# Performance work log

Measured on AMD Instinct MI355X. Metric: run time of the kernel, lower is better.

## Reference

```python
import jax, jax.numpy as jnp
import numpy as np

BN_EPS = 1e-5

def _bn_eval(x, gamma, beta):
    # Fresh torch BatchNorm1d in eval mode: running_mean=0, running_var=1
    return x * (gamma / jnp.sqrt(1.0 + BN_EPS)) + beta

def setup_inputs() -> dict:
    key = jax.random.key(0)
    ks = jax.random.split(key, 10)
    Q, K, H, W, D = 64, 128, 24, 8, 128
    L = H * W            # seq_len = 192
    FF = 2048            # dim_feedforward
    q_feat = jax.random.normal(ks[0], (Q, H, W, D), dtype=jnp.float32)
    g_feat = jax.random.normal(ks[1], (K, H, W, D), dtype=jnp.float32)
    se = jax.random.normal(ks[2], (L, L), dtype=jnp.float32)
    score_embed = (se + se.T).reshape(1, 1, L, L)
    s = 1.0 / np.sqrt(D)
    fc0_w = jax.random.uniform(ks[3], (D, D), jnp.float32, -s, s)
    fc0_b = jax.random.uniform(ks[4], (D,), jnp.float32, -s, s)
    s2 = 1.0 / np.sqrt(L)
    fc2_w = jax.random.uniform(ks[5], (FF, L), jnp.float32, -s2, s2)
    fc2_b = jax.random.uniform(ks[6], (FF,), jnp.float32, -s2, s2)
    s3 = 1.0 / np.sqrt(FF)
    fc3_w = jax.random.uniform(ks[7], (1, FF), jnp.float32, -s3, s3)
    fc3_b = jax.random.uniform(ks[8], (1,), jnp.float32, -s3, s3)
    bn1_g = jnp.ones((1,)); bn1_b = jnp.zeros((1,))
    bn2_g = jnp.ones((FF,)) + 0.1 * jax.random.normal(ks[9], (FF,), jnp.float32)
    bn2_b = jnp.zeros((FF,))
    bn3_g = jnp.ones((1,)); bn3_b = jnp.zeros((1,))
    return dict(q_feat=q_feat, g_feat=g_feat, score_embed=score_embed,
                fc0_w=fc0_w, fc0_b=fc0_b, fc2_w=fc2_w, fc2_b=fc2_b,
                fc3_w=fc3_w, fc3_b=fc3_b, bn1_g=bn1_g, bn1_b=bn1_b,
                bn2_g=bn2_g, bn2_b=bn2_b, bn3_g=bn3_g, bn3_b=bn3_b)

def reference(q_feat, g_feat, score_embed, fc0_w, fc0_b, fc2_w, fc2_b,
              fc3_w, fc3_b, bn1_g, bn1_b, bn2_g, bn2_b, bn3_g, bn3_b):
    Q = q_feat.shape[0]
    K = g_feat.shape[0]
    D = q_feat.shape[-1]
    L = score_embed.shape[-1]  # seq_len
    tgt = q_feat.reshape(Q, L, D)
    mem = g_feat.reshape(K, L, D)
    query = tgt @ fc0_w.T + fc0_b      # [Q, L, D]
    key_ = mem @ fc0_w.T + fc0_b       # [K, L, D]
    # [Q, K, L(s), L(t)] score, modulated by broadcast sigmoid bias
    score = jnp.einsum('qtd,ksd->qkst', query, key_) * jax.nn.sigmoid(score_embed)
    score = score.reshape(Q * K, L, L)
    # max over s and over t, concatenated per pair -> [QK, 2L]
    score = jnp.concatenate([score.max(axis=1), score.max(axis=2)], axis=-1)
    score = score.reshape(-1, L)       # [2*QK, L]
    score = _bn_eval(score, bn1_g, bn1_b)
    score = score @ fc2_w.T + fc2_b    # [2*QK, FF]
    score = _bn_eval(score, bn2_g, bn2_b)
    score = jax.nn.relu(score)
    score = score @ fc3_w.T + fc3_b    # [2*QK, 1]
    score = score.reshape(-1, 2).sum(axis=-1, keepdims=True)  # [QK, 1]
    score = _bn_eval(score, bn3_g, bn3_b)
    return score.reshape(Q, K)
```

## Files before the change

kernel.cpp:

```cpp
#include <hip/hip_runtime.h>

#define LL 192
#define FF 2048

typedef __attribute__((__ext_vector_type__(8)))  __bf16 bf16x8;
typedef __attribute__((__ext_vector_type__(4)))  __bf16 bf16x4;
typedef __attribute__((__ext_vector_type__(4)))  float  f32x4;

#define MFMA16(a, b, c) __builtin_amdgcn_mfma_f32_16x16x32_bf16((a), (b), (c), 0, 0, 0)


__launch_bounds__(256, 2)
__global__ void proj_prep_kernel(const float* __restrict__ qf_in,
                                 const float* __restrict__ gf_in,
                                 const float* __restrict__ fc0w,
                                 const float* __restrict__ fc0b,
                                 const float* __restrict__ se,
                                 const float* __restrict__ fc2w,
                                 const float* __restrict__ fc2b,
                                 const float* __restrict__ bn2g,
                                 const float* __restrict__ bn2b,
                                 const float* __restrict__ fc3w,
                                 __bf16* __restrict__ kfragA,
                                 __bf16* __restrict__ qfrag16,
                                 __bf16* __restrict__ sig16,
                                 __bf16* __restrict__ fc2w_bf,
                                 float* __restrict__ h2,
                                 float* __restrict__ bb2,
                                 float* __restrict__ f3)
{
    int bx = blockIdx.x, tid = threadIdx.x;
    if (bx >= 1152) {
        int i0 = (bx - 1152) * 256 + tid;
        const int stride = 160 * 256;
        const float c1 = rsqrtf(1.f + 1e-5f);
        for (int i = i0; i < LL * LL; i += stride) {
            int r = i & 3, lane = (i >> 2) & 63, tile = i >> 8;
            int jt = tile % 12, st = tile / 12;
            int s = st * 16 + (lane >> 4) * 4 + r;
            int t = jt * 16 + (lane & 15);
            sig16[i] = (__bf16)(1.f / (1.f + __expf(-se[s * 192 + t])));
        }
        for (int i = i0; i < FF * LL; i += stride)
            fc2w_bf[i] = (__bf16)fc2w[i];
        for (int i = i0; i < FF; i += stride) {
            float h = bn2g[i] * c1;
            h2[i]  = h;
            bb2[i] = fc2b[i] * h + bn2b[i];
            f3[i]  = fc3w[i];
        }
        return;
    }
    __shared__ __bf16 Xs[32][136];
    __shared__ __bf16 Ws[128][136];
    __shared__ __bf16 Os[4096];
    const float* src = (bx < 384) ? (qf_in + (size_t)bx * (32 * 128))
                                  : (gf_in + (size_t)(bx - 384) * (32 * 128));
#pragma unroll
    for (int it = 0; it < 4; ++it) {
        int e = (it * 256 + tid) * 4;
        int r = e >> 7, c = e & 127;
        float4 v = *reinterpret_cast<const float4*>(src + e);
        bf16x4 xv;
        xv[0] = (__bf16)v.x; xv[1] = (__bf16)v.y;
        xv[2] = (__bf16)v.z; xv[3] = (__bf16)v.w;
        *reinterpret_cast<bf16x4*>(&Xs[r][c]) = xv;
    }
#pragma unroll
    for (int it = 0; it < 16; ++it) {
        int e = (it * 256 + tid) * 4;
        int r = e >> 7, c = e & 127;
        float4 v = *reinterpret_cast<const float4*>(fc0w + e);
        bf16x4 xv;
        xv[0] = (__bf16)v.x; xv[1] = (__bf16)v.y;
        xv[2] = (__bf16)v.z; xv[3] = (__bf16)v.w;
        *reinterpret_cast<bf16x4*>(&Ws[r][c]) = xv;
    }
    __syncthreads();

    int wv = tid >> 6, lane = tid & 63, quad = lane >> 4, l16 = lane & 15;
    int n0 = wv * 32;
    f32x4 acc[2][2];
#pragma unroll
    for (int m = 0; m < 2; ++m)
#pragma unroll
        for (int n = 0; n < 2; ++n) acc[m][n] = (f32x4){0.f, 0.f, 0.f, 0.f};
#pragma unroll
    for (int ks = 0; ks < 4; ++ks) {
        bf16x8 a0 = *reinterpret_cast<const bf16x8*>(&Xs[l16][ks * 32 + quad * 8]);
        bf16x8 a1 = *reinterpret_cast<const bf16x8*>(&Xs[16 + l16][ks * 32 + quad * 8]);
        bf16x8 b0 = *reinterpret_cast<const bf16x8*>(&Ws[n0 + l16][ks * 32 + quad * 8]);
        bf16x8 b1 = *reinterpret_cast<const bf16x8*>(&Ws[n0 + 16 + l16][ks * 32 + quad * 8]);
        acc[0][0] = MFMA16(a0, b0, acc[0][0]);
        acc[0][1] = MFMA16(a0, b1, acc[0][1]);
        acc[1][0] = MFMA16(a1, b0, acc[1][0]);
        acc[1][1] = MFMA16(a1, b1, acc[1][1]);
    }
#pragma unroll
    for (int mt = 0; mt < 2; ++mt)
#pragma unroll
        for (int nt = 0; nt < 2; ++nt) {
            int d = n0 + nt * 16 + l16;
            float bv = fc0b[d];
            int abase = mt * 2048 + (d >> 5) * 512 + ((d >> 3) & 3) * 128 + (d & 7);
#pragma unroll
            for (int r = 0; r < 4; ++r)
                Os[abase + (quad * 4 + r) * 8] = (__bf16)(acc[mt][nt][r] + bv);
        }
    __syncthreads();

    int row0 = bx * 32;
    __bf16* dst;
    if (bx < 384) {
        int qi = row0 / 192, tg0 = (row0 % 192) >> 4;
        dst = qfrag16 + qi * 24576 + tg0 * 2048;
    } else {
        int rk0 = row0 - 12288;
        int ki = rk0 / 192, sg0 = (rk0 % 192) >> 4;
        dst = kfragA + ki * 24576 + sg0 * 2048;
    }
#pragma unroll
    for (int it = 0; it < 2; ++it) {
        int e = (it * 256 + tid) * 8;
        *reinterpret_cast<bf16x8*>(dst + e) =
            *reinterpret_cast<const bf16x8*>(&Os[e]);
    }
}

__launch_bounds__(256, 2)
__global__ void score_kernel(const __bf16* __restrict__ kfragA,
                             const __bf16* __restrict__ qfrag16,
                             const __bf16* __restrict__ sig16,
                             const float* __restrict__ bn1g,
                             const float* __restrict__ bn1b,
                             __bf16* __restrict__ Sred)
{
    __shared__ __bf16 Abuf[12288];
    __shared__ __bf16 rowT4[16][200];

    int tid = threadIdx.x;
    int q = blockIdx.x & 63;
    int kbase = (blockIdx.x >> 6) << 3;
    int w = tid >> 6, lane = tid & 63, quad = lane >> 4, l16 = lane & 15;
    const float g1c = bn1g[0] * rsqrtf(1.f + 1e-5f);
    const float b1v = bn1b[0];

    bf16x8 Bf[3][4];
    {
        const __bf16* qb = qfrag16 + (size_t)q * 24576 + lane * 8;
#pragma unroll
        for (int j = 0; j < 3; ++j)
#pragma unroll
            for (int ks = 0; ks < 4; ++ks)
                Bf[j][ks] = *reinterpret_cast<const bf16x8*>(
                    qb + ((3 * w + j) * 4 + ks) * 512);
    }

#pragma unroll 1
    for (int kk = 0; kk < 8; ++kk) {
        int kidx = kbase + kk;
        const __bf16* kp = kfragA + (size_t)kidx * 24576;
        size_t ob = (size_t)(q * 128 + kidx) * 384;
        float cm0 = -3.0e38f, cm1 = -3.0e38f, cm2 = -3.0e38f;

#pragma unroll 1
        for (int h = 0; h < 2; ++h) {
#pragma unroll
            for (int it = 0; it < 6; ++it) {
                int e = (it * 256 + tid) * 8;
                *reinterpret_cast<bf16x8*>(&Abuf[e]) =
                    *reinterpret_cast<const bf16x8*>(kp + 12288 * h + e);
            }
            __syncthreads();

#pragma unroll 1
            for (int lsc = 0; lsc < 3; ++lsc) {
                f32x4 acc[2][3];
#pragma unroll
                for (int i = 0; i < 2; ++i)
#pragma unroll
                    for (int j = 0; j < 3; ++j)
                        acc[i][j] = (f32x4){0.f, 0.f, 0.f, 0.f};

#pragma unroll
                for (int ks = 0; ks < 4; ++ks) {
                    bf16x8 a0 = *reinterpret_cast<const bf16x8*>(
                        &Abuf[((lsc * 2 + 0) * 4 + ks) * 512 + lane * 8]);
                    bf16x8 a1 = *reinterpret_cast<const bf16x8*>(
                        &Abuf[((lsc * 2 + 1) * 4 + ks) * 512 + lane * 8]);
#pragma unroll
                    for (int j = 0; j < 3; ++j) {
                        acc[0][j] = MFMA16(a0, Bf[j][ks], acc[0][j]);
                        acc[1][j] = MFMA16(a1, Bf[j][ks], acc[1][j]);
                    }
                }

#pragma unroll
                for (int i = 0; i < 2; ++i) {
                    int stile = 6 * h + lsc * 2 + i;
                    float rm0 = -3.0e38f, rm1 = -3.0e38f, rm2 = -3.0e38f, rm3 = -3.0e38f;
#pragma unroll
                    for (int j = 0; j < 3; ++j) {
                        bf16x4 sv = *reinterpret_cast<const bf16x4*>(
                            sig16 + ((size_t)(stile * 12 + 3 * w + j) * 64
                                     + lane) * 4);
                        float v0 = acc[i][j][0] * (float)sv[0];
                        float v1 = acc[i][j][1] * (float)sv[1];
                        float v2 = acc[i][j][2] * (float)sv[2];
                        float v3 = acc[i][j][3] * (float)sv[3];
                        rm0 = fmaxf(rm0, v0); rm1 = fmaxf(rm1, v1);
                        rm2 = fmaxf(rm2, v2); rm3 = fmaxf(rm3, v3);
                        float cj = fmaxf(fmaxf(v0, v1), fmaxf(v2, v3));
                        if (j == 0) cm0 = fmaxf(cm0, cj);
                        else if (j == 1) cm1 = fmaxf(cm1, cj);
                        else cm2 = fmaxf(cm2, cj);
                    }
                    rm0 = fmaxf(rm0, __shfl_xor(rm0, 1, 64));
                    rm0 = fmaxf(rm0, __shfl_xor(rm0, 2, 64));
                    rm1 = fmaxf(rm1, __shfl_xor(rm1, 1, 64));
                    rm1 = fmaxf(rm1, __shfl_xor(rm1, 2, 64));
                    rm2 = fmaxf(rm2, __shfl_xor(rm2, 1, 64));
                    rm2 = fmaxf(rm2, __shfl_xor(rm2, 2, 64));
                    rm3 = fmaxf(rm3, __shfl_xor(rm3, 1, 64));
                    rm3 = fmaxf(rm3, __shfl_xor(rm3, 2, 64));
                    if ((l16 & 3) == 0) {
                        bf16x4 pk;
                        pk[0] = (__bf16)rm0; pk[1] = (__bf16)rm1;
                        pk[2] = (__bf16)rm2; pk[3] = (__bf16)rm3;
                        *reinterpret_cast<bf16x4*>(
                            &rowT4[(l16 >> 2) * 4 + w]
                                  [96 * h + lsc * 32 + 16 * i + quad * 4]) = pk;
                    }
                }
            }
            __syncthreads();
        }

        {
            float v0 = cm0, v1 = cm1, v2 = cm2;
            v0 = fmaxf(v0, __shfl_xor(v0, 16, 64));
            v0 = fmaxf(v0, __shfl_xor(v0, 32, 64));
            v1 = fmaxf(v1, __shfl_xor(v1, 16, 64));
            v1 = fmaxf(v1, __shfl_xor(v1, 32, 64));
            v2 = fmaxf(v2, __shfl_xor(v2, 16, 64));
            v2 = fmaxf(v2, __shfl_xor(v2, 32, 64));
            if (quad == 0) {
                Sred[ob + (3 * w + 0) * 16 + l16] = (__bf16)(v0 * g1c + b1v);
                Sred[ob + (3 * w + 1) * 16 + l16] = (__bf16)(v1 * g1c + b1v);
                Sred[ob + (3 * w + 2) * 16 + l16] = (__bf16)(v2 * g1c + b1v);
            }
        }

        if (tid < 192) {
            float m1 = -3.0e38f;
#pragma unroll
            for (int c = 0; c < 16; ++c)
                m1 = fmaxf(m1, (float)rowT4[c][tid]);
            Sred[ob + 192 + tid] = (__bf16)(m1 * g1c + b1v);
        }
    }
}

__launch_bounds__(512, 1)
__global__ void mlp_kernel(const __bf16* __restrict__ Sred,
                           const __bf16* __restrict__ fc2w_bf,
                           const float* __restrict__ h2,
                           const float* __restrict__ bb2,
                           const float* __restrict__ f3,
                           const float* __restrict__ fc3b,
                           const float* __restrict__ bn3g,
                           const float* __restrict__ bn3b,
                           float* __restrict__ out)
{
    __shared__ __bf16 As[64][200];
    __shared__ float  psum_lds[8][64];
    int bx = blockIdx.x, tid = threadIdx.x;
    const __bf16* asrc = Sred + (size_t)bx * (64 * 192);
#pragma unroll
    for (int it = 0; it < 3; ++it) {
        int e = (it * 512 + tid) * 8;
        int r = e / 192, c = e - r * 192;
        *reinterpret_cast<bf16x8*>(&As[r][c]) =
            *reinterpret_cast<const bf16x8*>(asrc + e);
    }
    __syncthreads();

    int wv = tid >> 6, lane = tid & 63, quad = lane >> 4, l16 = lane & 15;
    bf16x8 af[4][6];
#pragma unroll
    for (int m = 0; m < 4; ++m)
#pragma unroll
        for (int kk = 0; kk < 6; ++kk)
            af[m][kk] = *reinterpret_cast<const bf16x8*>(
                &As[m * 16 + l16][kk * 32 + quad * 8]);

    float ps[4][4] = {{0.f,0.f,0.f,0.f},{0.f,0.f,0.f,0.f},
                      {0.f,0.f,0.f,0.f},{0.f,0.f,0.f,0.f}};
    for (int nt = 0; nt < 16; ++nt) {
        int n0 = wv * 256 + nt * 16;
        f32x4 acc[4];
#pragma unroll
        for (int m = 0; m < 4; ++m) acc[m] = (f32x4){0.f, 0.f, 0.f, 0.f};
        const __bf16* bp = fc2w_bf + (size_t)(n0 + l16) * 192 + quad * 8;
#pragma unroll
        for (int kk = 0; kk < 6; ++kk) {
            bf16x8 b = *reinterpret_cast<const bf16x8*>(bp + kk * 32);
#pragma unroll
            for (int m = 0; m < 4; ++m) acc[m] = MFMA16(af[m][kk], b, acc[m]);
        }
        int n = n0 + l16;
        float hh = h2[n], bb = bb2[n], ffv = f3[n];
#pragma unroll
        for (int m = 0; m < 4; ++m)
#pragma unroll
            for (int r = 0; r < 4; ++r)
                ps[m][r] += fmaxf(acc[m][r] * hh + bb, 0.f) * ffv;
    }
#pragma unroll
    for (int m = 0; m < 4; ++m)
#pragma unroll
        for (int r = 0; r < 4; ++r) {
            float v = ps[m][r];
            v += __shfl_xor(v, 1, 64);
            v += __shfl_xor(v, 2, 64);
            v += __shfl_xor(v, 4, 64);
            v += __shfl_xor(v, 8, 64);
            if (l16 == 0) psum_lds[wv][m * 16 + quad * 4 + r] = v;
        }
    __syncthreads();
    if (tid < 32) {
        float s = 0.f;
#pragma unroll
        for (int w = 0; w < 8; ++w)
            s += psum_lds[w][2 * tid] + psum_lds[w][2 * tid + 1];
        const float c1 = rsqrtf(1.f + 1e-5f);
        out[bx * 32 + tid] = (s + 2.f * fc3b[0]) * (bn3g[0] * c1) + bn3b[0];
    }
}

extern "C" void kernel_launch(void* const* d_in, const int* in_sizes, int n_in,
                              void* d_out, int out_size, void* d_ws, size_t ws_size,
                              hipStream_t stream)
{
    const float* q_feat = (const float*)d_in[0];
    const float* g_feat = (const float*)d_in[1];
    const float* se     = (const float*)d_in[2];
    const float* fc0w   = (const float*)d_in[3];
    const float* fc0b   = (const float*)d_in[4];
    const float* fc2w   = (const float*)d_in[5];
    const float* fc2b   = (const float*)d_in[6];
    const float* fc3w   = (const float*)d_in[7];
    const float* fc3b   = (const float*)d_in[8];
    const float* bn1g   = (const float*)d_in[9];
    const float* bn1b   = (const float*)d_in[10];
    const float* bn2g   = (const float*)d_in[11];
    const float* bn2b   = (const float*)d_in[12];
    const float* bn3g   = (const float*)d_in[13];
    const float* bn3b   = (const float*)d_in[14];
    float* out = (float*)d_out;

    char* ws = (char*)d_ws;
    __bf16* kfragA   = (__bf16*)(ws);
    __bf16* qfrag16  = (__bf16*)(ws +  6291456);
    __bf16* sig16    = (__bf16*)(ws +  9437184);
    __bf16* fc2w_bf  = (__bf16*)(ws +  9543680);
    float*  h2       = (float*) (ws + 10330112);
    float*  bb2      = (float*) (ws + 10338304);
    float*  f3       = (float*) (ws + 10346496);
    __bf16* Sred     = (__bf16*)(ws + 10354688);

    proj_prep_kernel<<<1312, 256, 0, stream>>>(q_feat, g_feat, fc0w, fc0b, se,
                                               fc2w, fc2b, bn2g, bn2b, fc3w,
                                               kfragA, qfrag16, sig16, fc2w_bf,
                                               h2, bb2, f3);
    score_kernel<<<1024, 256, 0, stream>>>(kfragA, qfrag16, sig16, bn1g, bn1b, Sred);
    mlp_kernel<<<256, 512, 0, stream>>>(Sred, fc2w_bf, h2, bb2, f3,
                                        fc3b, bn3g, bn3b, out);
}
```

Before: 229.6 us.

## Halve keys per score block, shrink LDS staging, store sigmoid bias in fp32

Result: no change. 228.9 us (-0.3%).

```diff
diff --git a/kernel.cpp b/kernel.cpp
--- a/kernel.cpp
+++ b/kernel.cpp
@@ -23,7 +23,7 @@
                                  const float* __restrict__ fc3w,
                                  __bf16* __restrict__ kfragA,
                                  __bf16* __restrict__ qfrag16,
-                                 __bf16* __restrict__ sig16,
+                                 float* __restrict__ sig32,
                                  __bf16* __restrict__ fc2w_bf,
                                  float* __restrict__ h2,
                                  float* __restrict__ bb2,
@@ -39,7 +39,7 @@
             int jt = tile % 12, st = tile / 12;
             int s = st * 16 + (lane >> 4) * 4 + r;
             int t = jt * 16 + (lane & 15);
-            sig16[i] = (__bf16)(1.f / (1.f + __expf(-se[s * 192 + t])));
+            sig32[i] = 1.f / (1.f + __expf(-se[s * 192 + t]));
         }
         for (int i = i0; i < FF * LL; i += stride)
             fc2w_bf[i] = (__bf16)fc2w[i];
@@ -130,17 +130,17 @@
 __launch_bounds__(256, 2)
 __global__ void score_kernel(const __bf16* __restrict__ kfragA,
                              const __bf16* __restrict__ qfrag16,
-                             const __bf16* __restrict__ sig16,
+                             const float* __restrict__ sig32,
                              const float* __restrict__ bn1g,
                              const float* __restrict__ bn1b,
                              __bf16* __restrict__ Sred)
 {
-    __shared__ __bf16 Abuf[12288];
+    __shared__ __bf16 Abuf[8192];
     __shared__ __bf16 rowT4[16][200];
 
     int tid = threadIdx.x;
     int q = blockIdx.x & 63;
-    int kbase = (blockIdx.x >> 6) << 3;
+    int kbase = (blockIdx.x >> 6) << 2;
     int w = tid >> 6, lane = tid & 63, quad = lane >> 4, l16 = lane & 15;
     const float g1c = bn1g[0] * rsqrtf(1.f + 1e-5f);
     const float b1v = bn1b[0];
@@ -157,24 +157,24 @@
     }
 
 #pragma unroll 1
-    for (int kk = 0; kk < 8; ++kk) {
+    for (int kk = 0; kk < 4; ++kk) {
         int kidx = kbase + kk;
         const __bf16* kp = kfragA + (size_t)kidx * 24576;
         size_t ob = (size_t)(q * 128 + kidx) * 384;
         float cm0 = -3.0e38f, cm1 = -3.0e38f, cm2 = -3.0e38f;
 
 #pragma unroll 1
-        for (int h = 0; h < 2; ++h) {
-#pragma unroll
-            for (int it = 0; it < 6; ++it) {
+        for (int h = 0; h < 3; ++h) {
+#pragma unroll
+            for (int it = 0; it < 4; ++it) {
                 int e = (it * 256 + tid) * 8;
                 *reinterpret_cast<bf16x8*>(&Abuf[e]) =
-                    *reinterpret_cast<const bf16x8*>(kp + 12288 * h + e);
+                    *reinterpret_cast<const bf16x8*>(kp + 8192 * h + e);
             }
             __syncthreads();
 
 #pragma unroll 1
-            for (int lsc = 0; lsc < 3; ++lsc) {
+            for (int lsc = 0; lsc < 2; ++lsc) {
                 f32x4 acc[2][3];
 #pragma unroll
                 for (int i = 0; i < 2; ++i)
@@ -197,24 +197,25 @@
 
 #pragma unroll
                 for (int i = 0; i < 2; ++i) {
-                    int stile = 6 * h + lsc * 2 + i;
-                    float rm0 = -3.0e38f, rm1 = -3.0e38f, rm2 = -3.0e38f, rm3 = -3.0e38f;
-#pragma unroll
-                    for (int j = 0; j < 3; ++j) {
-                        bf16x4 sv = *reinterpret_cast<const bf16x4*>(
-                            sig16 + ((size_t)(stile * 12 + 3 * w + j) * 64
-                                     + lane) * 4);
-                        float v0 = acc[i][j][0] * (float)sv[0];
-                        float v1 = acc[i][j][1] * (float)sv[1];
-                        float v2 = acc[i][j][2] * (float)sv[2];
-                        float v3 = acc[i][j][3] * (float)sv[3];
-                        rm0 = fmaxf(rm0, v0); rm1 = fmaxf(rm1, v1);
-                        rm2 = fmaxf(rm2, v2); rm3 = fmaxf(rm3, v3);
-                        float cj = fmaxf(fmaxf(v0, v1), fmaxf(v2, v3));
-                        if (j == 0) cm0 = fmaxf(cm0, cj);
-                        else if (j == 1) cm1 = fmaxf(cm1, cj);
-                        else cm2 = fmaxf(cm2, cj);
-                    }
+                    int stile = 4 * h + lsc * 2 + i;
+                    const float* sp = sig32 +
+                        ((size_t)(stile * 12 + 3 * w) * 64 + lane) * 4;
+                    f32x4 s0 = *reinterpret_cast<const f32x4*>(sp);
+                    f32x4 s1 = *reinterpret_cast<const f32x4*>(sp + 256);
+                    f32x4 s2 = *reinterpret_cast<const f32x4*>(sp + 512);
+                    float v00 = acc[i][0][0] * s0[0], v01 = acc[i][0][1] * s0[1];
+                    float v02 = acc[i][0][2] * s0[2], v03 = acc[i][0][3] * s0[3];
+                    float v10 = acc[i][1][0] * s1[0], v11 = acc[i][1][1] * s1[1];
+                    float v12 = acc[i][1][2] * s1[2], v13 = acc[i][1][3] * s1[3];
+                    float v20 = acc[i][2][0] * s2[0], v21 = acc[i][2][1] * s2[1];
+                    float v22 = acc[i][2][2] * s2[2], v23 = acc[i][2][3] * s2[3];
+                    float rm0 = fmaxf(fmaxf(v00, v10), v20);
+                    float rm1 = fmaxf(fmaxf(v01, v11), v21);
+                    float rm2 = fmaxf(fmaxf(v02, v12), v22);
+                    float rm3 = fmaxf(fmaxf(v03, v13), v23);
+                    cm0 = fmaxf(cm0, fmaxf(fmaxf(fmaxf(v00, v01), v02), v03));
+                    cm1 = fmaxf(cm1, fmaxf(fmaxf(fmaxf(v10, v11), v12), v13));
+                    cm2 = fmaxf(cm2, fmaxf(fmaxf(fmaxf(v20, v21), v22), v23));
                     rm0 = fmaxf(rm0, __shfl_xor(rm0, 1, 64));
                     rm0 = fmaxf(rm0, __shfl_xor(rm0, 2, 64));
                     rm1 = fmaxf(rm1, __shfl_xor(rm1, 1, 64));
@@ -229,7 +230,7 @@
                         pk[2] = (__bf16)rm2; pk[3] = (__bf16)rm3;
                         *reinterpret_cast<bf16x4*>(
                             &rowT4[(l16 >> 2) * 4 + w]
-                                  [96 * h + lsc * 32 + 16 * i + quad * 4]) = pk;
+                                  [stile * 16 + quad * 4]) = pk;
                     }
                 }
             }
@@ -362,18 +363,18 @@
     char* ws = (char*)d_ws;
     __bf16* kfragA   = (__bf16*)(ws);
     __bf16* qfrag16  = (__bf16*)(ws +  6291456);
-    __bf16* sig16    = (__bf16*)(ws +  9437184);
-    __bf16* fc2w_bf  = (__bf16*)(ws +  9543680);
-    float*  h2       = (float*) (ws + 10330112);
-    float*  bb2      = (float*) (ws + 10338304);
-    float*  f3       = (float*) (ws + 10346496);
-    __bf16* Sred     = (__bf16*)(ws + 10354688);
+    float*  sig32    = (float*) (ws +  9437184);
+    __bf16* fc2w_bf  = (__bf16*)(ws +  9584640);
+    float*  h2       = (float*) (ws + 10371072);
+    float*  bb2      = (float*) (ws + 10379264);
+    float*  f3       = (float*) (ws + 10387456);
+    __bf16* Sred     = (__bf16*)(ws + 10395648);
 
     proj_prep_kernel<<<1312, 256, 0, stream>>>(q_feat, g_feat, fc0w, fc0b, se,
                                                fc2w, fc2b, bn2g, bn2b, fc3w,
-                                               kfragA, qfrag16, sig16, fc2w_bf,
+                                               kfragA, qfrag16, sig32, fc2w_bf,
                                                h2, bb2, f3);
-    score_kernel<<<1024, 256, 0, stream>>>(kfragA, qfrag16, sig16, bn1g, bn1b, Sred);
+    score_kernel<<<2048, 256, 0, stream>>>(kfragA, qfrag16, sig32, bn1g, bn1b, Sred);
     mlp_kernel<<<256, 512, 0, stream>>>(Sred, fc2w_bf, h2, bb2, f3,
                                         fc3b, bn3g, bn3b, out);
 }
```
